# Kernel optimization log

Measured on AMD Instinct MI355X. Metric: run time of the kernel, lower is better.

Reference implementation:

```python
import jax, jax.numpy as jnp
import numpy as np

INV_SCALE = 1.0 / (0.5 * 9)  # module's inv_scale_factor; qk is DIVIDED by this (i.e. * 4.5)


def setup_inputs() -> dict:
    key0 = jax.random.key(0)
    ks = jax.random.split(key0, 8)
    B, Sq, Sk, D, Dv = 8, 2048, 2048, 128, 256
    return {
        "query": jax.random.normal(ks[0], (B, Sq, D), dtype=jnp.float32),
        "key": jax.random.normal(ks[1], (B, Sk, D), dtype=jnp.float32),
        "value": jax.random.normal(ks[2], (B, Sk, Dv), dtype=jnp.float32),
        "mask": jax.random.normal(ks[3], (B, Sq, Sk), dtype=jnp.float32),
        # Linear weights stored torch-style as [out_features, in_features]
        "W0": jax.random.normal(ks[4], (D, D), dtype=jnp.float32) * (1.0 / np.sqrt(D)),
        "W1": jax.random.normal(ks[5], (D, D), dtype=jnp.float32) * (1.0 / np.sqrt(D)),
        "W2": jax.random.normal(ks[6], (D, Dv), dtype=jnp.float32) * (1.0 / np.sqrt(Dv)),
        "Wout": jax.random.normal(ks[7], (Dv, D), dtype=jnp.float32) * (1.0 / np.sqrt(D)),
    }


def reference(query, key, value, mask, W0, W1, W2, Wout):
    r1 = jnp.einsum("bqd,od->bqo", query, W0)          # [B,Sq,128]
    r2 = jnp.einsum("bkd,od->bko", key, W1)            # [B,Sk,128]
    r3 = jnp.einsum("bkv,ov->bko", value, W2)          # [B,Sk,128]
    qk = jnp.einsum("bqd,bkd->bqk", r1, r2)            # [B,Sq,Sk]
    scaled_qk = qk / INV_SCALE
    softmax_qk = jax.nn.softmax(scaled_qk, axis=-1)
    # dropout is identity in eval mode (deterministic reference)
    v1 = jnp.einsum("bqk,bko->bqo", softmax_qk, r3)    # [B,Sq,128]
    v2 = jnp.einsum("bqo,vo->bqv", v1, Wout)           # [B,Sq,256]
    output = v2 + jnp.einsum("bqk,bkv->bqv", mask, value)
    return output
```

## Files before the change

### kernel.cpp

```cpp
#include <hip/hip_runtime.h>
#include <cstdint>

typedef __attribute__((ext_vector_type(8))) __bf16 bf16x8;
typedef __attribute__((ext_vector_type(4))) __bf16 bf16x4;
typedef __attribute__((ext_vector_type(4))) float f32x4;

#define MFMA16(a, b, c) __builtin_amdgcn_mfma_f32_16x16x32_bf16((a), (b), (c), 0, 0, 0)
#define WAITV(N) asm volatile("s_waitcnt vmcnt(" #N ")" ::: "memory")

static constexpr int SEQ = 2048;
static constexpr int DV = 256;
static constexpr float QK_SCALE = 4.5f;

__device__ __forceinline__ bf16x4 cvt4(float4 v) {
    bf16x4 y;
    y[0] = (__bf16)v.x; y[1] = (__bf16)v.y; y[2] = (__bf16)v.z; y[3] = (__bf16)v.w;
    return y;
}

__device__ __forceinline__ void gl_lds16(const void* g, void* l) {
    __builtin_amdgcn_global_load_lds((const __attribute__((address_space(1))) uint32_t*)g,
                                     (__attribute__((address_space(3))) uint32_t*)l, 16, 0, 0);
}

template <int K, int TRANS>
__global__ __launch_bounds__(256) void k_proj(const float* __restrict__ X,
                                              const float* __restrict__ W,
                                              __bf16* __restrict__ out,
                                              float outScale) {
    __shared__ __bf16 ldsX[64][136];
    __shared__ __bf16 ldsW[128][136];

    const int t = threadIdx.x;
    const int m0 = blockIdx.x * 64;
    const int w = t >> 6, l = t & 63, lrow = l & 15, lq = l >> 4;

    f32x4 acc[8];
#pragma unroll
    for (int i = 0; i < 8; ++i) acc[i] = f32x4{0.f, 0.f, 0.f, 0.f};

#pragma unroll
    for (int kh = 0; kh < K / 128; ++kh) {
        if (kh) __syncthreads();
#pragma unroll
        for (int i = 0; i < 8; ++i) {
            int idx = t + i * 256;
            int r = idx >> 5, c4 = idx & 31;
            float4 v = *(const float4*)(X + (size_t)(m0 + r) * K + kh * 128 + c4 * 4);
            *(bf16x4*)&ldsX[r][c4 * 4] = cvt4(v);
        }
#pragma unroll
        for (int i = 0; i < 16; ++i) {
            int idx = t + i * 256;
            int r = idx >> 5, c4 = idx & 31;
            float4 v = *(const float4*)(W + (size_t)r * K + kh * 128 + c4 * 4);
            *(bf16x4*)&ldsW[r][c4 * 4] = cvt4(v);
        }
        __syncthreads();

        bf16x8 aA[4];
#pragma unroll
        for (int kc = 0; kc < 4; ++kc)
            aA[kc] = *(const bf16x8*)((const char*)&ldsX[w * 16 + lrow][0] + kc * 64 + lq * 16);
#pragma unroll
        for (int nt = 0; nt < 8; ++nt) {
#pragma unroll
            for (int kc = 0; kc < 4; ++kc) {
                bf16x8 bB = *(const bf16x8*)((const char*)&ldsW[nt * 16 + lrow][0] + kc * 64 + lq * 16);
                acc[nt] = MFMA16(aA[kc], bB, acc[nt]);
            }
        }
    }

#pragma unroll
    for (int nt = 0; nt < 8; ++nt) {
        if (TRANS) {
            int gm = m0 + w * 16 + lq * 4;
            int b = gm >> 11, s = gm & 2047;
            int col = nt * 16 + lrow;
            int kt = s >> 5, s32 = s & 31;
            int slot = (s32 >> 3) ^ ((col >> 1) & 3);
            bf16x4 y;
#pragma unroll
            for (int j = 0; j < 4; ++j) y[j] = (__bf16)(acc[nt][j] * outScale);
            *(bf16x4*)(out + (((size_t)b * 64 + kt) * 128 + col) * 32 + slot * 8 + (s32 & 7)) = y;
        } else {
#pragma unroll
            for (int j = 0; j < 4; ++j) {
                int gm = m0 + w * 16 + lq * 4 + j;
                int col = nt * 16 + lrow;
                out[(size_t)gm * 128 + col] = (__bf16)(acc[nt][j] * outScale);
            }
        }
    }
}

__global__ __launch_bounds__(256) void k_vt(const float* __restrict__ V, __bf16* __restrict__ vt) {
    __shared__ __bf16 tile[64][72];
    const int t = threadIdx.x;
    const int b = blockIdx.z, s0 = blockIdx.x * 64, v0 = blockIdx.y * 64;
#pragma unroll
    for (int i = 0; i < 4; ++i) {
        int idx = t + i * 256;
        int r = idx >> 4, c4 = idx & 15;
        float4 x = *(const float4*)(V + ((size_t)b * SEQ + s0 + r) * DV + v0 + c4 * 4);
        *(bf16x4*)&tile[r][c4 * 4] = cvt4(x);
    }
    __syncthreads();
#pragma unroll
    for (int i = 0; i < 4; ++i) {
        int idx = t + i * 256;
        int vv = idx >> 4, c4 = idx & 15;
        bf16x4 y;
        y[0] = tile[c4 * 4 + 0][vv]; y[1] = tile[c4 * 4 + 1][vv];
        y[2] = tile[c4 * 4 + 2][vv]; y[3] = tile[c4 * 4 + 3][vv];
        int v = v0 + vv;
        int kt = (s0 >> 5) + (c4 >> 3);
        int slot = ((c4 >> 1) & 3) ^ ((v >> 1) & 3);
        *(bf16x4*)(vt + (((size_t)b * 64 + kt) * 256 + v) * 32 + slot * 8 + (c4 & 1) * 4) = y;
    }
}

__global__ __launch_bounds__(256) void k_cvt_bf16(const float* __restrict__ src,
                                                  __bf16* __restrict__ dst, int n4) {
    int i = blockIdx.x * 256 + threadIdx.x;
    if (i < n4) {
        float4 v = *(const float4*)(src + (size_t)i * 4);
        *(bf16x4*)(dst + (size_t)i * 4) = cvt4(v);
    }
}

__global__ __launch_bounds__(256) void k_flash(const __bf16* __restrict__ r1s,
                                               const __bf16* __restrict__ r2,
                                               const __bf16* __restrict__ r3p,
                                               __bf16* __restrict__ v1p,
                                               float* __restrict__ ml) {
    __shared__ __align__(16) __bf16 r2s[4][32 * 128];
    __shared__ __align__(16) __bf16 r3s[4][128 * 32];
    __shared__ __bf16 plds[4][16][48];

    const int t = threadIdx.x;
    const int bx = (int)((blockIdx.x & 7) * 64 + (blockIdx.x >> 3));
    const int b = bx >> 6, rem = bx & 63, q0 = (rem >> 1) * 64, kh = rem & 1;
    const int w = t >> 6, l = t & 63, lrow = l & 15, lq = l >> 4;

    const __bf16* r1b = r1s + (size_t)b * SEQ * 128;
    const __bf16* r2b = r2 + (size_t)b * SEQ * 128 + (size_t)kh * 1024 * 128;
    const __bf16* r3b = r3p + (size_t)b * 64 * 128 * 32 + (size_t)kh * 32 * 128 * 32;

    bf16x8 aQ[4];
    {
        const __bf16* p = r1b + (size_t)(q0 + w * 16 + lrow) * 128 + lq * 8;
#pragma unroll
        for (int kc = 0; kc < 4; ++kc) aQ[kc] = *(const bf16x8*)(p + kc * 32);
    }

    const __bf16* p_r2[2];
    const __bf16* p_r3[2];
#pragma unroll
    for (int q1 = 0; q1 < 2; ++q1) {
        int r = 8 * w + 4 * q1 + (l >> 4);
        int c = (l & 15) ^ (r & 15);
        p_r2[q1] = r2b + (size_t)r * 128 + c * 8;
        p_r3[q1] = r3b + (size_t)(2 * w + q1) * 512 + l * 8;
    }

    auto stage = [&](int bi) {
#pragma unroll
        for (int q1 = 0; q1 < 2; ++q1) {
            gl_lds16(p_r2[q1], &r2s[bi][(2 * w + q1) * 512]);
            gl_lds16(p_r3[q1], &r3s[bi][(2 * w + q1) * 512]);
            p_r2[q1] += 32 * 128;
            p_r3[q1] += 128 * 32;
        }
    };

    f32x4 acc[8];
#pragma unroll
    for (int i = 0; i < 8; ++i) acc[i] = f32x4{0.f, 0.f, 0.f, 0.f};
    float mrow[4] = {-INFINITY, -INFINITY, -INFINITY, -INFINITY};
    float lsum[4] = {0.f, 0.f, 0.f, 0.f};

    stage(0); stage(1); stage(2);
    for (int it = 0; it < 32; ++it) {
        if (it < 30) { WAITV(8); } else if (it == 30) { WAITV(4); } else { WAITV(0); }
        __builtin_amdgcn_s_barrier();
        __builtin_amdgcn_sched_barrier(0);
        if (it + 3 < 32) stage((it + 3) & 3);
        __builtin_amdgcn_sched_barrier(0);
        const __bf16* R2 = &r2s[it & 3][0];
        const __bf16* R3 = &r3s[it & 3][0];

        f32x4 sc[2];
#pragma unroll
        for (int ct = 0; ct < 2; ++ct) {
            f32x4 s = f32x4{0.f, 0.f, 0.f, 0.f};
#pragma unroll
            for (int kc = 0; kc < 4; ++kc) {
                int p = (kc * 4 + lq) ^ lrow;
                bf16x8 bb = *(const bf16x8*)&R2[(ct * 16 + lrow) * 128 + p * 8];
                s = MFMA16(aQ[kc], bb, s);
            }
            sc[ct] = s;
        }

        float pm[4], al[4];
#pragma unroll
        for (int j = 0; j < 4; ++j) pm[j] = fmaxf(sc[0][j], sc[1][j]);
#pragma unroll
        for (int off = 1; off <= 8; off <<= 1)
#pragma unroll
            for (int j = 0; j < 4; ++j) pm[j] = fmaxf(pm[j], __shfl_xor(pm[j], off, 64));
#pragma unroll
        for (int j = 0; j < 4; ++j) {
            float mn = fmaxf(mrow[j], pm[j]);
            al[j] = __expf(mrow[j] - mn);
            mrow[j] = mn;
        }
        float pr[2][4];
#pragma unroll
        for (int ct = 0; ct < 2; ++ct)
#pragma unroll
            for (int j = 0; j < 4; ++j)
                pr[ct][j] = __expf(sc[ct][j] - mrow[j]);
#pragma unroll
        for (int j = 0; j < 4; ++j)
            lsum[j] = lsum[j] * al[j] + pr[0][j] + pr[1][j];
#pragma unroll
        for (int ot = 0; ot < 8; ++ot)
#pragma unroll
            for (int j = 0; j < 4; ++j) acc[ot][j] *= al[j];

#pragma unroll
        for (int ct = 0; ct < 2; ++ct)
#pragma unroll
            for (int j = 0; j < 4; ++j)
                plds[w][lq * 4 + j][ct * 16 + lrow] = (__bf16)pr[ct][j];
        __builtin_amdgcn_s_waitcnt(0xc07f);
        bf16x8 pA = *(const bf16x8*)&plds[w][lrow][lq * 8];

#pragma unroll
        for (int ot = 0; ot < 8; ++ot) {
            int p = lq ^ ((lrow >> 1) & 3);
            bf16x8 bb = *(const bf16x8*)&R3[(ot * 16 + lrow) * 32 + p * 8];
            acc[ot] = MFMA16(pA, bb, acc[ot]);
        }
    }

#pragma unroll
    for (int off = 1; off <= 8; off <<= 1)
#pragma unroll
        for (int j = 0; j < 4; ++j) lsum[j] += __shfl_xor(lsum[j], off, 64);

    __bf16* vp = v1p + (size_t)kh * 8 * SEQ * 128;
#pragma unroll
    for (int ot = 0; ot < 8; ++ot)
#pragma unroll
        for (int j = 0; j < 4; ++j) {
            int q = q0 + w * 16 + lq * 4 + j;
            float v = acc[ot][j] / lsum[j];
            vp[((size_t)b * SEQ + q) * 128 + ot * 16 + lrow] = (__bf16)v;
        }
    if (lrow == 0) {
#pragma unroll
        for (int j = 0; j < 4; ++j) {
            size_t row = (size_t)b * SEQ + q0 + w * 16 + lq * 4 + j;
            ml[((size_t)kh * 8 * SEQ + row) * 2 + 0] = mrow[j];
            ml[((size_t)kh * 8 * SEQ + row) * 2 + 1] = lsum[j];
        }
    }
}

__global__ __launch_bounds__(256) void k_comb(const __bf16* __restrict__ v1p,
                                              const float* __restrict__ ml,
                                              __bf16* __restrict__ v1) {
    const int NROW = 8 * SEQ;
    int idx = blockIdx.x * 256 + threadIdx.x;
    int row = idx >> 4, c8 = (idx & 15) * 8;
    float m0 = ml[(size_t)row * 2 + 0], l0 = ml[(size_t)row * 2 + 1];
    float m1 = ml[((size_t)NROW + row) * 2 + 0], l1 = ml[((size_t)NROW + row) * 2 + 1];
    float M = fmaxf(m0, m1);
    float w0 = l0 * __expf(m0 - M), w1 = l1 * __expf(m1 - M);
    float inv = 1.f / (w0 + w1);
    w0 *= inv; w1 *= inv;
    bf16x8 a = *(const bf16x8*)(v1p + (size_t)row * 128 + c8);
    bf16x8 bb = *(const bf16x8*)(v1p + ((size_t)NROW + row) * 128 + c8);
    bf16x8 o;
#pragma unroll
    for (int j = 0; j < 8; ++j) o[j] = (__bf16)((float)a[j] * w0 + (float)bb[j] * w1);
    *(bf16x8*)(v1 + (size_t)row * 128 + c8) = o;
}

__global__ __launch_bounds__(512, 4) void k_out(const float* __restrict__ mask,
                                                const __bf16* __restrict__ vtp,
                                                const __bf16* __restrict__ v1,
                                                const __bf16* __restrict__ wob,
                                                float* __restrict__ out) {
    __shared__ __align__(16) __bf16 vbuf[3][256 * 32];
    __shared__ __align__(16) float mbuf[3][32 * 64];

    const int t = threadIdx.x;
    const int bid = (int)((blockIdx.x & 7) * 64 + (blockIdx.x >> 3));
    const int m0 = bid * 32;
    const int b = m0 >> 11, q0 = m0 & 2047;
    const int w = t >> 6, l = t & 63, lrow = l & 15, lq = l >> 4;
    const int rg = w & 1, cg = w >> 1;

    f32x4 acc[4];
#pragma unroll
    for (int i = 0; i < 4; ++i) acc[i] = f32x4{0.f, 0.f, 0.f, 0.f};

    const __bf16* vsrc[4];
    const float* msrc[2];
    if (w < 4) {
#pragma unroll
        for (int i = 0; i < 4; ++i)
            vsrc[i] = vtp + (size_t)b * 64 * 8192 + (w * 4 + i) * 512 + l * 8;
    } else {
        const int m = w - 4;
#pragma unroll
        for (int s = 0; s < 2; ++s) {
            int r = 4 * (m * 2 + s) + (l >> 4);
            int c = (l & 15) ^ (r & 7);
            msrc[s] = mask + ((size_t)(b * 2048 + q0 + r)) * 2048 + c * 4;
        }
    }

    if (w < 4) {
#pragma unroll
        for (int kt = 0; kt < 2; ++kt)
#pragma unroll
            for (int i = 0; i < 4; ++i)
                gl_lds16(vsrc[i] + (size_t)kt * 8192, &vbuf[kt][(w * 4 + i) * 512]);
    } else {
        const int m = w - 4;
#pragma unroll
        for (int s = 0; s < 2; ++s)
            gl_lds16(msrc[s], &mbuf[0][(m * 2 + s) * 256]);
    }

    for (int it = 0; it < 64; ++it) {
        if (w >= 4) {
            const int m = w - 4;
            if (it <= 61) {
                int e = (it >> 1) + 1, s = it & 1;
                gl_lds16(msrc[s] + (size_t)e * 64, &mbuf[e % 3][(m * 2 + s) * 256]);
            }
            if ((it & 1) == 0) {
                if (it <= 60) { WAITV(1); } else { WAITV(0); }
            }
        } else {
            if (it < 63) { WAITV(4); } else { WAITV(0); }
        }
        __builtin_amdgcn_s_barrier();
        __builtin_amdgcn_sched_barrier(0);
        if (w < 4 && it + 2 < 64) {
            int kt = it + 2;
#pragma unroll
            for (int i = 0; i < 4; ++i)
                gl_lds16(vsrc[i] + (size_t)kt * 8192, &vbuf[kt % 3][(w * 4 + i) * 512]);
        }
        __builtin_amdgcn_sched_barrier(0);

        const float* Mb = &mbuf[(it >> 1) % 3][0];
        const __bf16* V = &vbuf[it % 3][0];
        const int h = it & 1;
        int c0 = (h * 8 + lq * 2) ^ (lrow & 7);
        int c1 = (h * 8 + lq * 2 + 1) ^ (lrow & 7);
        float4 f0 = *(const float4*)&Mb[(rg * 16 + lrow) * 64 + c0 * 4];
        float4 f1 = *(const float4*)&Mb[(rg * 16 + lrow) * 64 + c1 * 4];
        bf16x8 aM;
        aM[0] = (__bf16)f0.x; aM[1] = (__bf16)f0.y; aM[2] = (__bf16)f0.z; aM[3] = (__bf16)f0.w;
        aM[4] = (__bf16)f1.x; aM[5] = (__bf16)f1.y; aM[6] = (__bf16)f1.z; aM[7] = (__bf16)f1.w;

        const int pv = lq ^ ((lrow >> 1) & 3);
#pragma unroll
        for (int vt8 = 0; vt8 < 4; ++vt8) {
            bf16x8 bb = *(const bf16x8*)&V[(cg * 64 + vt8 * 16 + lrow) * 32 + pv * 8];
            acc[vt8] = MFMA16(aM, bb, acc[vt8]);
        }
    }

    bf16x8 aV[4];
#pragma unroll
    for (int oc = 0; oc < 4; ++oc)
        aV[oc] = *(const bf16x8*)(v1 + (size_t)(m0 + rg * 16 + lrow) * 128 + oc * 32 + lq * 8);
#pragma unroll
    for (int vt8 = 0; vt8 < 4; ++vt8) {
#pragma unroll
        for (int oc = 0; oc < 4; ++oc) {
            bf16x8 bb = *(const bf16x8*)(wob + (size_t)(cg * 64 + vt8 * 16 + lrow) * 128 + oc * 32 + lq * 8);
            acc[vt8] = MFMA16(aV[oc], bb, acc[vt8]);
        }
    }

#pragma unroll
    for (int vt8 = 0; vt8 < 4; ++vt8)
#pragma unroll
        for (int j = 0; j < 4; ++j) {
            int gq = m0 + rg * 16 + lq * 4 + j;
            out[(size_t)gq * 256 + cg * 64 + vt8 * 16 + lrow] = acc[vt8][j];
        }
}

extern "C" void kernel_launch(void* const* d_in, const int* in_sizes, int n_in,
                              void* d_out, int out_size, void* d_ws, size_t ws_size,
                              hipStream_t stream) {
    const float* q    = (const float*)d_in[0];
    const float* k    = (const float*)d_in[1];
    const float* v    = (const float*)d_in[2];
    const float* mask = (const float*)d_in[3];
    const float* W0   = (const float*)d_in[4];
    const float* W1   = (const float*)d_in[5];
    const float* W2   = (const float*)d_in[6];
    const float* Wout = (const float*)d_in[7];
    float* out = (float*)d_out;

    char* ws = (char*)d_ws;
    __bf16* r1s = (__bf16*)(ws);
    __bf16* r2b = (__bf16*)(ws + (4ull << 20));
    __bf16* r3t = (__bf16*)(ws + (8ull << 20));
    __bf16* vtb = (__bf16*)(ws + (12ull << 20));
    __bf16* wob = (__bf16*)(ws + (20ull << 20));
    __bf16* v1b = (__bf16*)(ws + (21ull << 20));
    __bf16* v1p = (__bf16*)(ws + (25ull << 20));
    float*  mlb = (float*)(ws + (33ull << 20));

    k_proj<128, 0><<<256, 256, 0, stream>>>(q, W0, r1s, QK_SCALE);
    k_proj<128, 0><<<256, 256, 0, stream>>>(k, W1, r2b, 1.0f);
    k_proj<256, 1><<<256, 256, 0, stream>>>(v, W2, r3t, 1.0f);
    k_vt<<<dim3(32, 4, 8), 256, 0, stream>>>(v, vtb);
    k_cvt_bf16<<<32, 256, 0, stream>>>(Wout, wob, 8192);
    k_flash<<<512, 256, 0, stream>>>(r1s, r2b, r3t, v1p, mlb);
    k_comb<<<1024, 256, 0, stream>>>(v1p, mlb, v1b);
    k_out<<<512, 512, 0, stream>>>(mask, vtb, v1b, wob, out);
}
```

Measured before the change: 349.1 us.

## Merge preprocessing kernels, fold split-K combine into output kernel, deepen mask prefetch

```diff
diff --git a/kernel.cpp b/kernel.cpp
--- a/kernel.cpp
+++ b/kernel.cpp
@@ -24,15 +24,14 @@
 }
 
 template <int K, int TRANS>
-__global__ __launch_bounds__(256) void k_proj(const float* __restrict__ X,
-                                              const float* __restrict__ W,
-                                              __bf16* __restrict__ out,
-                                              float outScale) {
-    __shared__ __bf16 ldsX[64][136];
-    __shared__ __bf16 ldsW[128][136];
+__device__ __forceinline__ void proj_body(const float* __restrict__ X,
+                                          const float* __restrict__ W,
+                                          __bf16* __restrict__ out,
+                                          float outScale, int m0, char* smem) {
+    auto ldsX = (__bf16(*)[136])smem;
+    auto ldsW = (__bf16(*)[136])(smem + 64 * 136 * 2);
 
     const int t = threadIdx.x;
-    const int m0 = blockIdx.x * 64;
     const int w = t >> 6, l = t & 63, lrow = l & 15, lq = l >> 4;
 
     f32x4 acc[8];
@@ -95,10 +94,12 @@
     }
 }
 
-__global__ __launch_bounds__(256) void k_vt(const float* __restrict__ V, __bf16* __restrict__ vt) {
-    __shared__ __bf16 tile[64][72];
+__device__ __forceinline__ void vt_body(const float* __restrict__ V,
+                                        __bf16* __restrict__ vt, int wg, char* smem) {
+    auto tile = (__bf16(*)[72])smem;
     const int t = threadIdx.x;
-    const int b = blockIdx.z, s0 = blockIdx.x * 64, v0 = blockIdx.y * 64;
+    const int b = wg >> 7, by = (wg >> 5) & 3, bxx = wg & 31;
+    const int s0 = bxx * 64, v0 = by * 64;
 #pragma unroll
     for (int i = 0; i < 4; ++i) {
         int idx = t + i * 256;
@@ -121,12 +122,34 @@
     }
 }
 
-__global__ __launch_bounds__(256) void k_cvt_bf16(const float* __restrict__ src,
-                                                  __bf16* __restrict__ dst, int n4) {
-    int i = blockIdx.x * 256 + threadIdx.x;
-    if (i < n4) {
-        float4 v = *(const float4*)(src + (size_t)i * 4);
-        *(bf16x4*)(dst + (size_t)i * 4) = cvt4(v);
+__global__ __launch_bounds__(256) void k_pre(const float* __restrict__ q,
+                                             const float* __restrict__ k,
+                                             const float* __restrict__ v,
+                                             const float* __restrict__ W0,
+                                             const float* __restrict__ W1,
+                                             const float* __restrict__ W2,
+                                             const float* __restrict__ Wout,
+                                             __bf16* __restrict__ r1s,
+                                             __bf16* __restrict__ r2b,
+                                             __bf16* __restrict__ r3t,
+                                             __bf16* __restrict__ vtb,
+                                             __bf16* __restrict__ wob) {
+    __shared__ __align__(16) char smem[52224];
+    const int bx = blockIdx.x;
+    if (bx < 256) {
+        proj_body<128, 0>(q, W0, r1s, QK_SCALE, bx * 64, smem);
+    } else if (bx < 512) {
+        proj_body<128, 0>(k, W1, r2b, 1.0f, (bx - 256) * 64, smem);
+    } else if (bx < 768) {
+        proj_body<256, 1>(v, W2, r3t, 1.0f, (bx - 512) * 64, smem);
+    } else if (bx < 1792) {
+        vt_body(v, vtb, bx - 768, smem);
+    } else {
+        int i = (bx - 1792) * 256 + threadIdx.x;
+        if (i < 8192) {
+            float4 x = *(const float4*)(Wout + (size_t)i * 4);
+            *(bf16x4*)(wob + (size_t)i * 4) = cvt4(x);
+        }
     }
 }
 
@@ -271,33 +294,14 @@
     }
 }
 
-__global__ __launch_bounds__(256) void k_comb(const __bf16* __restrict__ v1p,
-                                              const float* __restrict__ ml,
-                                              __bf16* __restrict__ v1) {
-    const int NROW = 8 * SEQ;
-    int idx = blockIdx.x * 256 + threadIdx.x;
-    int row = idx >> 4, c8 = (idx & 15) * 8;
-    float m0 = ml[(size_t)row * 2 + 0], l0 = ml[(size_t)row * 2 + 1];
-    float m1 = ml[((size_t)NROW + row) * 2 + 0], l1 = ml[((size_t)NROW + row) * 2 + 1];
-    float M = fmaxf(m0, m1);
-    float w0 = l0 * __expf(m0 - M), w1 = l1 * __expf(m1 - M);
-    float inv = 1.f / (w0 + w1);
-    w0 *= inv; w1 *= inv;
-    bf16x8 a = *(const bf16x8*)(v1p + (size_t)row * 128 + c8);
-    bf16x8 bb = *(const bf16x8*)(v1p + ((size_t)NROW + row) * 128 + c8);
-    bf16x8 o;
-#pragma unroll
-    for (int j = 0; j < 8; ++j) o[j] = (__bf16)((float)a[j] * w0 + (float)bb[j] * w1);
-    *(bf16x8*)(v1 + (size_t)row * 128 + c8) = o;
-}
-
 __global__ __launch_bounds__(512, 4) void k_out(const float* __restrict__ mask,
                                                 const __bf16* __restrict__ vtp,
-                                                const __bf16* __restrict__ v1,
+                                                const __bf16* __restrict__ v1p,
+                                                const float* __restrict__ ml,
                                                 const __bf16* __restrict__ wob,
                                                 float* __restrict__ out) {
     __shared__ __align__(16) __bf16 vbuf[3][256 * 32];
-    __shared__ __align__(16) float mbuf[3][32 * 64];
+    __shared__ __align__(16) float mbuf[4][32 * 64];
 
     const int t = threadIdx.x;
     const int bid = (int)((blockIdx.x & 7) * 64 + (blockIdx.x >> 3));
@@ -335,19 +339,21 @@
     } else {
         const int m = w - 4;
 #pragma unroll
-        for (int s = 0; s < 2; ++s)
-            gl_lds16(msrc[s], &mbuf[0][(m * 2 + s) * 256]);
+        for (int e = 0; e < 2; ++e)
+#pragma unroll
+            for (int s = 0; s < 2; ++s)
+                gl_lds16(msrc[s] + (size_t)e * 64, &mbuf[e][(m * 2 + s) * 256]);
     }
 
     for (int it = 0; it < 64; ++it) {
         if (w >= 4) {
             const int m = w - 4;
-            if (it <= 61) {
-                int e = (it >> 1) + 1, s = it & 1;
-                gl_lds16(msrc[s] + (size_t)e * 64, &mbuf[e % 3][(m * 2 + s) * 256]);
+            if (it <= 59) {
+                int en = (it >> 1) + 2, s = it & 1;
+                gl_lds16(msrc[s] + (size_t)en * 64, &mbuf[en & 3][(m * 2 + s) * 256]);
             }
             if ((it & 1) == 0) {
-                if (it <= 60) { WAITV(1); } else { WAITV(0); }
+                if (it <= 58) { WAITV(3); } else if (it == 60) { WAITV(2); } else { WAITV(0); }
             }
         } else {
             if (it < 63) { WAITV(4); } else { WAITV(0); }
@@ -362,7 +368,7 @@
         }
         __builtin_amdgcn_sched_barrier(0);
 
-        const float* Mb = &mbuf[(it >> 1) % 3][0];
+        const float* Mb = &mbuf[(it >> 1) & 3][0];
         const __bf16* V = &vbuf[it % 3][0];
         const int h = it & 1;
         int c0 = (h * 8 + lq * 2) ^ (lrow & 7);
@@ -381,10 +387,24 @@
         }
     }
 
+    const int NROW = 8 * SEQ;
+    const int row = m0 + rg * 16 + lrow;
+    float am0 = ml[(size_t)row * 2 + 0], al0 = ml[(size_t)row * 2 + 1];
+    float am1 = ml[((size_t)NROW + row) * 2 + 0], al1 = ml[((size_t)NROW + row) * 2 + 1];
+    float M = fmaxf(am0, am1);
+    float w0 = al0 * __expf(am0 - M), w1 = al1 * __expf(am1 - M);
+    float inv = 1.f / (w0 + w1);
+    w0 *= inv; w1 *= inv;
     bf16x8 aV[4];
 #pragma unroll
-    for (int oc = 0; oc < 4; ++oc)
-        aV[oc] = *(const bf16x8*)(v1 + (size_t)(m0 + rg * 16 + lrow) * 128 + oc * 32 + lq * 8);
+    for (int oc = 0; oc < 4; ++oc) {
+        bf16x8 a = *(const bf16x8*)(v1p + (size_t)row * 128 + oc * 32 + lq * 8);
+        bf16x8 bh = *(const bf16x8*)(v1p + ((size_t)NROW + row) * 128 + oc * 32 + lq * 8);
+        bf16x8 o;
+#pragma unroll
+        for (int j = 0; j < 8; ++j) o[j] = (__bf16)((float)a[j] * w0 + (float)bh[j] * w1);
+        aV[oc] = o;
+    }
 #pragma unroll
     for (int vt8 = 0; vt8 < 4; ++vt8) {
 #pragma unroll
@@ -422,16 +442,10 @@
     __bf16* r3t = (__bf16*)(ws + (8ull << 20));
     __bf16* vtb = (__bf16*)(ws + (12ull << 20));
     __bf16* wob = (__bf16*)(ws + (20ull << 20));
-    __bf16* v1b = (__bf16*)(ws + (21ull << 20));
     __bf16* v1p = (__bf16*)(ws + (25ull << 20));
     float*  mlb = (float*)(ws + (33ull << 20));
 
-    k_proj<128, 0><<<256, 256, 0, stream>>>(q, W0, r1s, QK_SCALE);
-    k_proj<128, 0><<<256, 256, 0, stream>>>(k, W1, r2b, 1.0f);
-    k_proj<256, 1><<<256, 256, 0, stream>>>(v, W2, r3t, 1.0f);
-    k_vt<<<dim3(32, 4, 8), 256, 0, stream>>>(v, vtb);
-    k_cvt_bf16<<<32, 256, 0, stream>>>(Wout, wob, 8192);
+    k_pre<<<1824, 256, 0, stream>>>(q, k, v, W0, W1, W2, Wout, r1s, r2b, r3t, vtb, wob);
     k_flash<<<512, 256, 0, stream>>>(r1s, r2b, r3t, v1p, mlb);
-    k_comb<<<1024, 256, 0, stream>>>(v1p, mlb, v1b);
-    k_out<<<512, 512, 0, stream>>>(mask, vtb, v1b, wob, out);
-}
+    k_out<<<512, 512, 0, stream>>>(mask, vtb, v1p, mlb, wob, out);
+}
```

Result: faster. 335.1 us (-4.0%).
